# Kernel optimization log

Hardware: AMD Instinct MI355X
Metric: run time of the kernel (lower is better)

Reference implementation:

```python
import jax, jax.numpy as jnp
import numpy as np

N_NODES = 8192
N_EDGES = 524288
D_IN = 256
D_OUT = 256


def setup_inputs() -> dict:
    key = jax.random.key(0)
    ks = jax.random.split(key, 8)
    h = jax.random.normal(ks[0], (N_NODES, D_IN), dtype=jnp.float32)
    # Xavier-uniform-like scale for weights
    s = (6.0 / (D_IN + D_OUT)) ** 0.5
    W = jax.random.uniform(ks[1], (D_IN, D_OUT), jnp.float32, -s, s)
    Wq = jax.random.uniform(ks[2], (D_IN, D_OUT), jnp.float32, -s, s)
    bq = jnp.zeros((D_OUT,), jnp.float32)
    Wk = jax.random.uniform(ks[3], (D_IN, D_OUT), jnp.float32, -s, s)
    bk = jnp.zeros((D_OUT,), jnp.float32)
    senders = jax.random.randint(ks[4], (N_EDGES,), 0, N_NODES, dtype=jnp.int64 if jax.config.jax_enable_x64 else jnp.int32)
    receivers = jax.random.randint(ks[5], (N_EDGES,), 0, N_NODES, dtype=jnp.int64 if jax.config.jax_enable_x64 else jnp.int32)
    return {"h": h, "W": W, "Wq": Wq, "bq": bq, "Wk": Wk, "bk": bk,
            "senders": senders, "receivers": receivers}


def reference(h, W, Wq, bq, Wk, bk, senders, receivers):
    # Projected node features: (N, D_OUT)
    h_proj = jnp.dot(h, W)
    # Dense attention logits a = q @ k^T: (N, N), as in the original module
    q = jnp.dot(h, Wq) + bq
    k = jnp.dot(h, Wk) + bk
    a = jnp.dot(q, k.T)
    # Gather per-edge messages and attention weights, weight, scatter-add
    messages = h_proj[senders] * a[senders, receivers][:, None]  # (E, D_OUT)
    aggregated = jax.ops.segment_sum(messages, receivers, num_segments=h.shape[0])
    return jax.nn.relu(aggregated)
```

## Files before the change

### kernel.cpp

```cpp
#include <hip/hip_runtime.h>
#include <stdint.h>

typedef unsigned short u16;
typedef unsigned int u32;
typedef short v8s __attribute__((ext_vector_type(8)));
typedef float v4f __attribute__((ext_vector_type(4)));

#define N_NODES 8192
#define N_EDGES 524288
#define DFEAT 256
#define PAD 160

static __device__ __forceinline__ float bflo(u32 u) { return __uint_as_float(u << 16); }
static __device__ __forceinline__ float bfhi(u32 u) { return __uint_as_float(u & 0xffff0000u); }
static __device__ __forceinline__ u16 f2bf(float f) {
    u32 u = __float_as_uint(f);
    u32 r = (u + 0x7fffu + ((u >> 16) & 1u)) >> 16;
    return (u16)r;
}

__global__ void prep(const float* __restrict__ w0, const float* __restrict__ w1,
                     const float* __restrict__ w2,
                     const int* __restrict__ recv, const int* __restrict__ send,
                     u16* __restrict__ wt,
                     int* __restrict__ cnt, int* __restrict__ es_pad) {
    __shared__ u16 t[64][65];
    int b = blockIdx.x;
    if (b < 2048) {
        int e = b * 256 + threadIdx.x;
        int r = recv[e];
        int pos = atomicAdd(&cnt[r], 1);
        if (pos < PAD) es_pad[r * PAD + pos] = send[e];
    } else {
        int bb = b - 2048;
        int region = bb >> 4;
        int tile = bb & 15;
        int k0 = (tile >> 2) * 64, n0 = (tile & 3) * 64;
        const float* w = (region == 0) ? w0 : ((region == 1) ? w1 : w2);
        int tx = threadIdx.x & 63, ty = threadIdx.x >> 6;
#pragma unroll
        for (int it = 0; it < 16; it++) {
            int row = it * 4 + ty;
            t[row][tx] = f2bf(w[(k0 + row) * 256 + n0 + tx]);
        }
        __syncthreads();
        u16* o = wt + region * 65536;
#pragma unroll
        for (int it = 0; it < 16; it++) {
            int row = it * 4 + ty;
            o[(n0 + row) * 256 + k0 + tx] = t[tx][row];
        }
    }
}

__global__ __launch_bounds__(256) void gemm_proj(
    const float* __restrict__ h, const u16* __restrict__ wt,
    const float* __restrict__ bq, const float* __restrict__ bk,
    u16* __restrict__ hproj, u16* __restrict__ qb, u16* __restrict__ kb) {
    int wave = threadIdx.x >> 6;
    int lane = threadIdx.x & 63;
    int lm = lane & 15;
    int lq = lane >> 4;
    int m0 = blockIdx.x * 64 + wave * 16;
    int region = blockIdx.y >> 2;
    int n0b = (blockIdx.y & 3) * 64;
    const u16* wtr = wt + region * 65536;

    v4f acc[4];
#pragma unroll
    for (int nt = 0; nt < 4; nt++) acc[nt] = (v4f){0.f, 0.f, 0.f, 0.f};

    const float* arow = h + (m0 + lm) * 256 + lq * 8;
#pragma unroll
    for (int k0 = 0; k0 < 256; k0 += 32) {
        float4 u0 = *(const float4*)(arow + k0);
        float4 u1 = *(const float4*)(arow + k0 + 4);
        v8s a;
        a[0] = (short)f2bf(u0.x); a[1] = (short)f2bf(u0.y);
        a[2] = (short)f2bf(u0.z); a[3] = (short)f2bf(u0.w);
        a[4] = (short)f2bf(u1.x); a[5] = (short)f2bf(u1.y);
        a[6] = (short)f2bf(u1.z); a[7] = (short)f2bf(u1.w);
#pragma unroll
        for (int nt = 0; nt < 4; nt++) {
            v8s b = *(const v8s*)(wtr + (n0b + nt * 16 + lm) * 256 + k0 + lq * 8);
            acc[nt] = __builtin_amdgcn_mfma_f32_16x16x32_bf16(a, b, acc[nt], 0, 0, 0);
        }
    }

    u16* outp = (region == 0) ? hproj : ((region == 1) ? qb : kb);
    const float* bias = (region == 1) ? bq : ((region == 2) ? bk : nullptr);
#pragma unroll
    for (int nt = 0; nt < 4; nt++) {
        int n = n0b + nt * 16 + lm;
        float bv = bias ? bias[n] : 0.f;
#pragma unroll
        for (int i = 0; i < 4; i++) {
            int m = m0 + lq * 4 + i;
            outp[m * 256 + n] = f2bf(acc[nt][i] + bv);
        }
    }
}

__global__ __launch_bounds__(64) void edge_fused(
    const u16* __restrict__ qb, const u16* __restrict__ kb, const u16* __restrict__ hpb,
    const int* __restrict__ cnt, const int* __restrict__ es_pad,
    float* __restrict__ out) {
    __shared__ float sc[16];
    int lane = threadIdx.x;
    int r = blockIdx.x;
    int lm = lane & 15, lq = lane >> 4;
    int lh = lane & 31, half = lane >> 5;
    int n = min(cnt[r], PAD);
    int base = r * PAD;

    v8s kf[8];
    const u16* krow = kb + r * 256 + lq * 8;
#pragma unroll
    for (int t = 0; t < 8; t++) kf[t] = *(const v8s*)(krow + t * 32);

    float a[8];
#pragma unroll
    for (int i = 0; i < 8; i++) a[i] = 0.f;

    for (int c0 = 0; c0 < n; c0 += 16) {
        int jq = c0 + lm;
        if (jq >= n) jq = n - 1;
        int sq = es_pad[base + jq];
        const u16* qrow = qb + (long)sq * 256 + lq * 8;
        v4f acc = (v4f){0.f, 0.f, 0.f, 0.f};
#pragma unroll
        for (int t = 0; t < 8; t++) {
            v8s av = *(const v8s*)(qrow + t * 32);
            acc = __builtin_amdgcn_mfma_f32_16x16x32_bf16(av, kf[t], acc, 0, 0, 0);
        }
        if (lm == 0) {
#pragma unroll
            for (int i = 0; i < 4; i++) sc[lq * 4 + i] = acc[i];
        }
        __threadfence_block();

        int m = n - c0;
        if (m >= 16) {
#pragma unroll
            for (int u = 0; u < 8; u++) {
                int sh = __shfl(sq, 2 * u + half, 64);
                float p = sc[2 * u + half];
                uint4 hu = *(const uint4*)(hpb + (long)sh * 256 + lh * 8);
                a[0] += p * bflo(hu.x); a[1] += p * bfhi(hu.x);
                a[2] += p * bflo(hu.y); a[3] += p * bfhi(hu.y);
                a[4] += p * bflo(hu.z); a[5] += p * bfhi(hu.z);
                a[6] += p * bflo(hu.w); a[7] += p * bfhi(hu.w);
            }
        } else {
            for (int t = half; t < m; t += 2) {
                int sh = __shfl(sq, t, 64);
                float p = sc[t];
                uint4 hu = *(const uint4*)(hpb + (long)sh * 256 + lh * 8);
                a[0] += p * bflo(hu.x); a[1] += p * bfhi(hu.x);
                a[2] += p * bflo(hu.y); a[3] += p * bfhi(hu.y);
                a[4] += p * bflo(hu.z); a[5] += p * bfhi(hu.z);
                a[6] += p * bflo(hu.w); a[7] += p * bfhi(hu.w);
            }
        }
    }

#pragma unroll
    for (int i = 0; i < 8; i++) a[i] += __shfl_xor(a[i], 32, 64);

    if (half == 0) {
        float4 o0, o1;
        o0.x = fmaxf(a[0], 0.f); o0.y = fmaxf(a[1], 0.f);
        o0.z = fmaxf(a[2], 0.f); o0.w = fmaxf(a[3], 0.f);
        o1.x = fmaxf(a[4], 0.f); o1.y = fmaxf(a[5], 0.f);
        o1.z = fmaxf(a[6], 0.f); o1.w = fmaxf(a[7], 0.f);
        float* op = out + r * 256 + lh * 8;
        *(float4*)op = o0;
        *(float4*)(op + 4) = o1;
    }
}

extern "C" void kernel_launch(void* const* d_in, const int* in_sizes, int n_in,
                              void* d_out, int out_size, void* d_ws, size_t ws_size,
                              hipStream_t stream) {
    const float* h  = (const float*)d_in[0];
    const float* W  = (const float*)d_in[1];
    const float* Wq = (const float*)d_in[2];
    const float* bq = (const float*)d_in[3];
    const float* Wk = (const float*)d_in[4];
    const float* bk = (const float*)d_in[5];
    const int* senders   = (const int*)d_in[6];
    const int* receivers = (const int*)d_in[7];
    float* out = (float*)d_out;

    char* ws = (char*)d_ws;
    u16* wt     = (u16*)ws;
    u16* hproj  = (u16*)(ws + 393216);
    u16* qb     = hproj + N_NODES * DFEAT;
    u16* kb     = qb + N_NODES * DFEAT;
    int* cnt    = (int*)(kb + N_NODES * DFEAT);
    int* es_pad = cnt + N_NODES;

    hipMemsetAsync(cnt, 0, N_NODES * sizeof(int), stream);
    prep<<<2096, 256, 0, stream>>>(W, Wq, Wk, receivers, senders, wt, cnt, es_pad);
    gemm_proj<<<dim3(128, 12), 256, 0, stream>>>(h, wt, bq, bk, hproj, qb, kb);
    edge_fused<<<N_NODES, 64, 0, stream>>>(qb, kb, hproj, cnt, es_pad, out);
}
```

Measured before the change: 184.4 us.

## Split fused edge kernel into separate score and aggregation kernels

Splits the fused per-receiver edge kernel into two kernels. The first computes the attention scores with MFMA and writes them to a padded global buffer. The second gathers projected sender rows and accumulates them, with a simpler unrolled loop that has no LDS handoff or shuffles. This drops the serial dependency between the score MFMA and the gather inside one wave, at the cost of an extra launch and a round trip of the scores through global memory.

```diff
diff --git a/kernel.cpp b/kernel.cpp
--- a/kernel.cpp
+++ b/kernel.cpp
@@ -10,6 +10,7 @@
 #define N_EDGES 524288
 #define DFEAT 256
 #define PAD 160
+#define PADE 176
 
 static __device__ __forceinline__ float bflo(u32 u) { return __uint_as_float(u << 16); }
 static __device__ __forceinline__ float bfhi(u32 u) { return __uint_as_float(u & 0xffff0000u); }
@@ -101,26 +102,21 @@
     }
 }
 
-__global__ __launch_bounds__(64) void edge_fused(
-    const u16* __restrict__ qb, const u16* __restrict__ kb, const u16* __restrict__ hpb,
+__global__ __launch_bounds__(64) void edge_score(
+    const u16* __restrict__ qb, const u16* __restrict__ kb,
     const int* __restrict__ cnt, const int* __restrict__ es_pad,
-    float* __restrict__ out) {
-    __shared__ float sc[16];
+    float* __restrict__ ea_pad) {
     int lane = threadIdx.x;
     int r = blockIdx.x;
     int lm = lane & 15, lq = lane >> 4;
-    int lh = lane & 31, half = lane >> 5;
     int n = min(cnt[r], PAD);
     int base = r * PAD;
+    int obase = r * PADE;
 
     v8s kf[8];
     const u16* krow = kb + r * 256 + lq * 8;
 #pragma unroll
     for (int t = 0; t < 8; t++) kf[t] = *(const v8s*)(krow + t * 32);
-
-    float a[8];
-#pragma unroll
-    for (int i = 0; i < 8; i++) a[i] = 0.f;
 
     for (int c0 = 0; c0 < n; c0 += 16) {
         int jq = c0 + lm;
@@ -135,33 +131,38 @@
         }
         if (lm == 0) {
 #pragma unroll
-            for (int i = 0; i < 4; i++) sc[lq * 4 + i] = acc[i];
-        }
-        __threadfence_block();
-
-        int m = n - c0;
-        if (m >= 16) {
-#pragma unroll
-            for (int u = 0; u < 8; u++) {
-                int sh = __shfl(sq, 2 * u + half, 64);
-                float p = sc[2 * u + half];
-                uint4 hu = *(const uint4*)(hpb + (long)sh * 256 + lh * 8);
-                a[0] += p * bflo(hu.x); a[1] += p * bfhi(hu.x);
-                a[2] += p * bflo(hu.y); a[3] += p * bfhi(hu.y);
-                a[4] += p * bflo(hu.z); a[5] += p * bfhi(hu.z);
-                a[6] += p * bflo(hu.w); a[7] += p * bfhi(hu.w);
+            for (int i = 0; i < 4; i++) {
+                int row = c0 + lq * 4 + i;
+                ea_pad[obase + row] = acc[i];
             }
-        } else {
-            for (int t = half; t < m; t += 2) {
-                int sh = __shfl(sq, t, 64);
-                float p = sc[t];
-                uint4 hu = *(const uint4*)(hpb + (long)sh * 256 + lh * 8);
-                a[0] += p * bflo(hu.x); a[1] += p * bfhi(hu.x);
-                a[2] += p * bflo(hu.y); a[3] += p * bfhi(hu.y);
-                a[4] += p * bflo(hu.z); a[5] += p * bfhi(hu.z);
-                a[6] += p * bflo(hu.w); a[7] += p * bfhi(hu.w);
-            }
-        }
+        }
+    }
+}
+
+__global__ __launch_bounds__(64) void edge_aggregate(
+    const u16* __restrict__ hpb, const int* __restrict__ cnt,
+    const int* __restrict__ es_pad, const float* __restrict__ ea_pad,
+    float* __restrict__ out) {
+    int lane = threadIdx.x;
+    int r = blockIdx.x;
+    int lh = lane & 31, half = lane >> 5;
+    int n = min(cnt[r], PAD);
+    int base = r * PAD;
+    int obase = r * PADE;
+
+    float a[8];
+#pragma unroll
+    for (int i = 0; i < 8; i++) a[i] = 0.f;
+
+#pragma unroll 4
+    for (int t = half; t < n; t += 2) {
+        int s = es_pad[base + t];
+        float p = ea_pad[obase + t];
+        uint4 hu = *(const uint4*)(hpb + (long)s * 256 + lh * 8);
+        a[0] += p * bflo(hu.x); a[1] += p * bfhi(hu.x);
+        a[2] += p * bflo(hu.y); a[3] += p * bfhi(hu.y);
+        a[4] += p * bflo(hu.z); a[5] += p * bfhi(hu.z);
+        a[6] += p * bflo(hu.w); a[7] += p * bfhi(hu.w);
     }
 
 #pragma unroll
@@ -199,9 +200,11 @@
     u16* kb     = qb + N_NODES * DFEAT;
     int* cnt    = (int*)(kb + N_NODES * DFEAT);
     int* es_pad = cnt + N_NODES;
+    float* ea_pad = (float*)(es_pad + N_NODES * PAD);
 
     hipMemsetAsync(cnt, 0, N_NODES * sizeof(int), stream);
     prep<<<2096, 256, 0, stream>>>(W, Wq, Wk, receivers, senders, wt, cnt, es_pad);
     gemm_proj<<<dim3(128, 12), 256, 0, stream>>>(h, wt, bq, bk, hproj, qb, kb);
-    edge_fused<<<N_NODES, 64, 0, stream>>>(qb, kb, hproj, cnt, es_pad, out);
-}
+    edge_score<<<N_NODES, 64, 0, stream>>>(qb, kb, cnt, es_pad, ea_pad);
+    edge_aggregate<<<N_NODES, 64, 0, stream>>>(hproj, cnt, es_pad, ea_pad, out);
+}
```

Result: slower. 188.4 us (+2.1%).
